# Optimization experiments

Measured on AMD Instinct MI355X. Metric: run time of the kernel, lower is better.

Reference implementation:

```python
import jax, jax.numpy as jnp
import numpy as np


def setup_inputs() -> dict:
    key = jax.random.key(0)
    k1, k2, k3, k4 = jax.random.split(key, 4)
    B, S, D, F = 16, 4096, 1024, 1024
    x = jax.random.normal(k1, (B, S, D), dtype=jnp.float32)
    # Keras 'normal' initializer ~ N(0, 0.05); scale similarly for realism
    W_key = jax.random.normal(k2, (D, F), dtype=jnp.float32) * 0.05
    W_query = jax.random.normal(k3, (D, F), dtype=jnp.float32) * 0.05
    W_value = jax.random.normal(k4, (D, F), dtype=jnp.float32) * 0.05
    return {"x": x, "W_key": W_key, "W_query": W_query, "W_value": W_value}


def reference(x, W_key, W_query, W_value):
    # x: [B,S,D]; W_*: [D,F]
    keys = jnp.tanh(jnp.einsum("bsd,df->bsf", x, W_key))
    query = jnp.tanh(jnp.einsum("bsd,df->bsf", x, W_query))
    value = jnp.tanh(jnp.einsum("bsd,df->bsf", x, W_value))
    # diag(Q K^T) == per-token dot product, computed directly in O(S*F)
    attn_scores = jnp.einsum("bsf,bsf->bs", query, keys)  # [B,S]
    attn_softmax = jax.nn.softmax(attn_scores, axis=-1)[..., None]  # [B,S,1]
    # value^T @ softmax -> [B,F,1]
    weighted_input = jnp.einsum("bsf,bso->bfo", value, attn_softmax)
    return weighted_input, attn_softmax
```

## Files before the change

kernel.cpp:

```cpp
#include <hip/hip_runtime.h>
#include <hip/hip_bf16.h>
#include <math.h>
#include <stdint.h>

typedef _Float16 f16;
typedef _Float16 half8 __attribute__((ext_vector_type(8)));
typedef float f32x4 __attribute__((ext_vector_type(4)));

#define B_ 16
#define S_ 4096
#define D_ 1024
#define F_ 1024
#define TOK (B_*S_)
#define TB2 256
#define FB 128
#define NFB (F_/FB)
#define BK2 64
#define NT (D_/BK2)
#define NS 16
#define CS (S_/NS)

__device__ __forceinline__ void gload_lds16(const void* g, void* l) {
    __builtin_amdgcn_global_load_lds(
        (__attribute__((address_space(1))) const unsigned int*)(unsigned long long)(uintptr_t)g,
        (__attribute__((address_space(3))) unsigned int*)(unsigned int)(uintptr_t)l,
        16, 0, 0);
}

__device__ __forceinline__ void fma4(float4& a, float s, const float4& wv) {
    a.x += s * wv.x; a.y += s * wv.y; a.z += s * wv.z; a.w += s * wv.w;
}
__device__ __forceinline__ void wtanh4(float4& acc, float pw, const float4& a) {
    acc.x += pw * tanhf(a.x); acc.y += pw * tanhf(a.y);
    acc.z += pw * tanhf(a.z); acc.w += pw * tanhf(a.w);
}

__global__ void cvt_x(const float* __restrict__ x, f16* __restrict__ xh) {
    size_t i = ((size_t)blockIdx.x * 256 + threadIdx.x) * 8;
    float4 a = *(const float4*)(x + i);
    float4 b = *(const float4*)(x + i + 4);
    half8 h = {(f16)a.x,(f16)a.y,(f16)a.z,(f16)a.w,
               (f16)b.x,(f16)b.y,(f16)b.z,(f16)b.w};
    *(half8*)(xh + i) = h;
}

__global__ void cvt_w(const float* __restrict__ Wk, const float* __restrict__ Wq,
                      f16* __restrict__ wt) {
    __shared__ float tile[32][33];
    const float* W = (blockIdx.z == 0) ? Wk : Wq;
    f16* outp = wt + (size_t)blockIdx.z * D_ * F_;
    int x0 = blockIdx.x * 32, y0 = blockIdx.y * 32;
    int tx = threadIdx.x, ty = threadIdx.y;
#pragma unroll
    for (int i = 0; i < 4; i++)
        tile[ty + i*8][tx] = W[(size_t)(y0 + ty + i*8) * F_ + x0 + tx];
    __syncthreads();
#pragma unroll
    for (int i = 0; i < 4; i++)
        outp[(size_t)(x0 + ty + i*8) * D_ + y0 + tx] = (f16)tile[tx][ty + i*8];
}

__launch_bounds__(512, 2)
__global__ void score_gemm(const f16* __restrict__ xh, const f16* __restrict__ wt,
                           float* __restrict__ part) {
    __shared__ __align__(16) f16 Xs[2][TB2][BK2];
    __shared__ __align__(16) f16 Ks[2][FB][BK2];
    __shared__ __align__(16) f16 Qs[2][FB][BK2];
    __shared__ float sred[2][TB2];

    const int f0   = blockIdx.x * FB;
    const int tok0 = blockIdx.y * TB2;
    const int t    = threadIdx.x;
    const int lane = t & 63;
    const int w    = t >> 6;
    const int wr   = (w >> 1) * 64;
    const int wc   = (w & 1) * 64;

    const f16* wK = wt + (size_t)f0 * D_;
    const f16* wQ = wt + (size_t)D_ * F_ + (size_t)f0 * D_;

#define STAGE(bi, k0) do {                                                         \
        char* xb = (char*)Xs[bi] + w * 1024;                                       \
        char* kb = (char*)Ks[bi] + w * 1024;                                       \
        char* qb = (char*)Qs[bi] + w * 1024;                                       \
        _Pragma("unroll")                                                          \
        for (int i_ = 0; i_ < 4; ++i_) {                                           \
            int c_ = i_ * 512 + t;                                                 \
            gload_lds16(xh + (size_t)(tok0 + (c_ >> 3)) * D_ + (k0) + (c_ & 7) * 8,\
                        xb + i_ * 8192);                                           \
        }                                                                          \
        _Pragma("unroll")                                                          \
        for (int i_ = 0; i_ < 2; ++i_) {                                           \
            int c_ = i_ * 512 + t;                                                 \
            gload_lds16(wK + (size_t)(c_ >> 3) * D_ + (k0) + (c_ & 7) * 8,         \
                        kb + i_ * 8192);                                           \
            gload_lds16(wQ + (size_t)(c_ >> 3) * D_ + (k0) + (c_ & 7) * 8,         \
                        qb + i_ * 8192);                                           \
        }                                                                          \
    } while (0)

    f32x4 accQ[4][4] = {};
    f32x4 accK[4][4] = {};

    STAGE(0, 0);
    __syncthreads();
    int cur = 0;

    for (int kt = 0; kt < NT; ++kt) {
        if (kt + 1 < NT) STAGE(cur ^ 1, (kt + 1) * BK2);

#pragma unroll
        for (int ks = 0; ks < 2; ++ks) {
            half8 aF[4], bKf[4], bQf[4];
#pragma unroll
            for (int m = 0; m < 4; ++m)
                aF[m] = *(const half8*)&Xs[cur][wr + m * 16 + (lane & 15)][ks * 32 + (lane >> 4) * 8];
#pragma unroll
            for (int n = 0; n < 4; ++n) {
                bKf[n] = *(const half8*)&Ks[cur][wc + n * 16 + (lane & 15)][ks * 32 + (lane >> 4) * 8];
                bQf[n] = *(const half8*)&Qs[cur][wc + n * 16 + (lane & 15)][ks * 32 + (lane >> 4) * 8];
            }
#pragma unroll
            for (int n = 0; n < 4; ++n)
#pragma unroll
                for (int m = 0; m < 4; ++m) {
                    accK[m][n] = __builtin_amdgcn_mfma_f32_16x16x32_f16(aF[m], bKf[n], accK[m][n], 0, 0, 0);
                    accQ[m][n] = __builtin_amdgcn_mfma_f32_16x16x32_f16(aF[m], bQf[n], accQ[m][n], 0, 0, 0);
                }
        }
        __syncthreads();
        cur ^= 1;
    }
#undef STAGE

#pragma unroll
    for (int m = 0; m < 4; ++m) {
        float s[4] = {0.f, 0.f, 0.f, 0.f};
#pragma unroll
        for (int n = 0; n < 4; ++n)
#pragma unroll
            for (int j = 0; j < 4; ++j)
                s[j] += tanhf(accQ[m][n][j]) * tanhf(accK[m][n][j]);
#pragma unroll
        for (int j = 0; j < 4; ++j) {
            s[j] += __shfl_xor(s[j], 1);
            s[j] += __shfl_xor(s[j], 2);
            s[j] += __shfl_xor(s[j], 4);
            s[j] += __shfl_xor(s[j], 8);
        }
        if ((lane & 15) == 0) {
            int g = lane >> 4;
#pragma unroll
            for (int j = 0; j < 4; ++j)
                sred[w & 1][wr + m * 16 + g * 4 + j] = s[j];
        }
    }
    __syncthreads();
    if (t < TB2)
        part[(size_t)blockIdx.x * TOK + tok0 + t] = sred[0][t] + sred[1][t];
}

__global__ void softmax_k(const float* __restrict__ part, float* __restrict__ out) {
    __shared__ float sc[S_];
    __shared__ float red[256];
    const int b = blockIdx.x, t = threadIdx.x;
    float lmax = -1e30f;
    for (int i = t; i < S_; i += 256) {
        float s = 0.f;
#pragma unroll
        for (int fb = 0; fb < NFB; ++fb) s += part[(size_t)fb * TOK + b * S_ + i];
        sc[i] = s;
        lmax = fmaxf(lmax, s);
    }
    red[t] = lmax; __syncthreads();
    for (int o = 128; o > 0; o >>= 1) { if (t < o) red[t] = fmaxf(red[t], red[t + o]); __syncthreads(); }
    const float mx = red[0]; __syncthreads();
    float lsum = 0.f;
    for (int i = t; i < S_; i += 256) { float e = expf(sc[i] - mx); sc[i] = e; lsum += e; }
    red[t] = lsum; __syncthreads();
    for (int o = 128; o > 0; o >>= 1) { if (t < o) red[t] += red[t + o]; __syncthreads(); }
    const float inv = 1.0f / red[0];
    for (int i = t; i < S_; i += 256)
        out[(size_t)B_ * F_ + (size_t)b * S_ + i] = sc[i] * inv;
}

__launch_bounds__(256)
__global__ void value_k3(const float* __restrict__ x, const float* __restrict__ Wv,
                         const float* __restrict__ p_in, float* __restrict__ vpart) {
    __shared__ __align__(16) float xs[4][D_];
    __shared__ float ps[CS];
    __shared__ int   idxs[CS];
    __shared__ int   wsum[4];
    const int b = blockIdx.x, c = blockIdx.y;
    const int t = threadIdx.x, lane = t & 63, w = t >> 6;
    const int s0 = c * CS;

    float p = p_in[(size_t)b * S_ + s0 + t];
    bool flag = p > 1e-7f;
    unsigned long long mask = __ballot(flag);
    if (lane == 0) wsum[w] = __popcll(mask);
    __syncthreads();
    int base = 0;
#pragma unroll
    for (int i = 0; i < 4; ++i) if (i < w) base += wsum[i];
    const int cnt = wsum[0] + wsum[1] + wsum[2] + wsum[3];
    if (flag) {
        int pos = base + __popcll(mask & ((1ull << lane) - 1ull));
        idxs[pos] = s0 + t;
        ps[pos] = p;
    }
    __syncthreads();

    float4 acc = {0.f, 0.f, 0.f, 0.f};
    for (int g = 0; g < cnt; g += 4) {
        __syncthreads();
#pragma unroll
        for (int r = 0; r < 4; ++r) {
            float4 v = {0.f, 0.f, 0.f, 0.f};
            if (g + r < cnt)
                v = ((const float4*)(x + ((size_t)b * S_ + idxs[g + r]) * D_))[t];
            ((float4*)xs[r])[t] = v;
        }
        __syncthreads();
        float4 a0 = {0,0,0,0}, a1 = {0,0,0,0}, a2 = {0,0,0,0}, a3 = {0,0,0,0};
#pragma unroll 2
        for (int dq = 0; dq < D_ / 4; ++dq) {
            const float* wr = Wv + (size_t)dq * 4 * F_;
            float4 wv0 = ((const float4*)(wr        ))[t];
            float4 wv1 = ((const float4*)(wr + F_   ))[t];
            float4 wv2 = ((const float4*)(wr + 2*F_ ))[t];
            float4 wv3 = ((const float4*)(wr + 3*F_ ))[t];
            float4 x0 = ((const float4*)xs[0])[dq];
            float4 x1 = ((const float4*)xs[1])[dq];
            float4 x2 = ((const float4*)xs[2])[dq];
            float4 x3 = ((const float4*)xs[3])[dq];
            fma4(a0, x0.x, wv0); fma4(a0, x0.y, wv1); fma4(a0, x0.z, wv2); fma4(a0, x0.w, wv3);
            fma4(a1, x1.x, wv0); fma4(a1, x1.y, wv1); fma4(a1, x1.z, wv2); fma4(a1, x1.w, wv3);
            fma4(a2, x2.x, wv0); fma4(a2, x2.y, wv1); fma4(a2, x2.z, wv2); fma4(a2, x2.w, wv3);
            fma4(a3, x3.x, wv0); fma4(a3, x3.y, wv1); fma4(a3, x3.z, wv2); fma4(a3, x3.w, wv3);
        }
        int rem = cnt - g;
        if (rem > 0) wtanh4(acc, ps[g + 0], a0);
        if (rem > 1) wtanh4(acc, ps[g + 1], a1);
        if (rem > 2) wtanh4(acc, ps[g + 2], a2);
        if (rem > 3) wtanh4(acc, ps[g + 3], a3);
    }
    ((float4*)(vpart + ((size_t)c * B_ + b) * F_))[t] = acc;
}

__global__ void value_red(const float* __restrict__ vpart, float* __restrict__ out) {
    int i = blockIdx.x * 256 + threadIdx.x;
    float s = 0.f;
#pragma unroll
    for (int c = 0; c < NS; ++c) s += vpart[(size_t)c * B_ * F_ + i];
    out[i] = s;
}

extern "C" void kernel_launch(void* const* d_in, const int* in_sizes, int n_in,
                              void* d_out, int out_size, void* d_ws, size_t ws_size,
                              hipStream_t stream) {
    const float* x  = (const float*)d_in[0];
    const float* Wk = (const float*)d_in[1];
    const float* Wq = (const float*)d_in[2];
    const float* Wv = (const float*)d_in[3];
    float* out = (float*)d_out;
    char* ws = (char*)d_ws;

    f16*   xh   = (f16*)ws;
    f16*   wt   = (f16*)(ws + (size_t)TOK * D_ * 2);
    float* part = (float*)(ws + (size_t)TOK * D_ * 2 + 2 * (size_t)D_ * F_ * 2);

    cvt_x<<<TOK * D_ / 8 / 256, 256, 0, stream>>>(x, xh);
    cvt_w<<<dim3(32, 32, 2), dim3(32, 8), 0, stream>>>(Wk, Wq, wt);
    score_gemm<<<dim3(NFB, TOK / TB2), 512, 0, stream>>>(xh, wt, part);
    softmax_k<<<B_, 256, 0, stream>>>(part, out);
    float* vpart = part;
    const float* p_in = out + (size_t)B_ * F_;
    value_k3<<<dim3(B_, NS), 256, 0, stream>>>(x, Wv, p_in, vpart);
    value_red<<<B_ * F_ / 256, 256, 0, stream>>>(vpart, out);
}
```

Measured before the change: 649.9 us.

## Deepen score GEMM pipeline to four LDS stages with swizzle and block remap

Rewrites the score GEMM main loop to use a 4-slot LDS ring with K-step 32 and three tiles in flight, waited on with explicit vmcnt counts and a single barrier per step. X and weight loads are split so they interleave with the K and Q MFMA groups, and MFMA sections run at raised wave priority. An XOR swizzle on the LDS layout is meant to avoid bank conflicts, and block indices are remapped so that consecutive blocks share the same token tile for L2 reuse. The manual vmcnt accounting is fragile, and halving the K step doubles the number of barriers.

```diff
diff --git a/kernel.cpp b/kernel.cpp
--- a/kernel.cpp
+++ b/kernel.cpp
@@ -15,8 +15,8 @@
 #define TB2 256
 #define FB 128
 #define NFB (F_/FB)
-#define BK2 64
-#define NT (D_/BK2)
+#define BK3 32
+#define NT3 (D_/BK3)
 #define NS 16
 #define CS (S_/NS)
 
@@ -63,13 +63,17 @@
 __launch_bounds__(512, 2)
 __global__ void score_gemm(const f16* __restrict__ xh, const f16* __restrict__ wt,
                            float* __restrict__ part) {
-    __shared__ __align__(16) f16 Xs[2][TB2][BK2];
-    __shared__ __align__(16) f16 Ks[2][FB][BK2];
-    __shared__ __align__(16) f16 Qs[2][FB][BK2];
+    __shared__ __align__(16) f16 Xs[4][TB2 * BK3];
+    __shared__ __align__(16) f16 Ks[4][FB * BK3];
+    __shared__ __align__(16) f16 Qs[4][FB * BK3];
     __shared__ float sred[2][TB2];
 
-    const int f0   = blockIdx.x * FB;
-    const int tok0 = blockIdx.y * TB2;
+    const int hid  = blockIdx.x + blockIdx.y * NFB;
+    const int orig = (hid & 7) * 256 + (hid >> 3);
+    const int fb   = orig & 7;
+    const int f0   = fb * FB;
+    const int tok0 = (orig >> 3) * TB2;
+
     const int t    = threadIdx.x;
     const int lane = t & 63;
     const int w    = t >> 6;
@@ -79,59 +83,100 @@
     const f16* wK = wt + (size_t)f0 * D_;
     const f16* wQ = wt + (size_t)D_ * F_ + (size_t)f0 * D_;
 
-#define STAGE(bi, k0) do {                                                         \
-        char* xb = (char*)Xs[bi] + w * 1024;                                       \
-        char* kb = (char*)Ks[bi] + w * 1024;                                       \
-        char* qb = (char*)Qs[bi] + w * 1024;                                       \
-        _Pragma("unroll")                                                          \
-        for (int i_ = 0; i_ < 4; ++i_) {                                           \
-            int c_ = i_ * 512 + t;                                                 \
-            gload_lds16(xh + (size_t)(tok0 + (c_ >> 3)) * D_ + (k0) + (c_ & 7) * 8,\
-                        xb + i_ * 8192);                                           \
-        }                                                                          \
-        _Pragma("unroll")                                                          \
-        for (int i_ = 0; i_ < 2; ++i_) {                                           \
-            int c_ = i_ * 512 + t;                                                 \
-            gload_lds16(wK + (size_t)(c_ >> 3) * D_ + (k0) + (c_ & 7) * 8,         \
-                        kb + i_ * 8192);                                           \
-            gload_lds16(wQ + (size_t)(c_ >> 3) * D_ + (k0) + (c_ & 7) * 8,         \
-                        qb + i_ * 8192);                                           \
-        }                                                                          \
+    const int cX0 = t, cX1 = t + 512;
+    const int rX0 = cX0 >> 2, rX1 = cX1 >> 2;
+    const int qX0 = (cX0 & 3) ^ ((rX0 >> 1) & 3);
+    const int qX1 = (cX1 & 3) ^ ((rX1 >> 1) & 3);
+    const f16* srcX0 = xh + (size_t)(tok0 + rX0) * D_ + qX0 * 8;
+    const f16* srcX1 = xh + (size_t)(tok0 + rX1) * D_ + qX1 * 8;
+    const int rW = t >> 2;
+    const int qW = (t & 3) ^ ((rW >> 1) & 3);
+    const f16* srcK = wK + (size_t)rW * D_ + qW * 8;
+    const f16* srcQ = wQ + (size_t)rW * D_ + qW * 8;
+    const int wbase = w * 1024;
+
+    int offA[4], offB[4];
+#pragma unroll
+    for (int m = 0; m < 4; ++m) {
+        int row = wr + m * 16 + (lane & 15);
+        int q   = (lane >> 4) ^ ((row >> 1) & 3);
+        offA[m] = row * 32 + q * 8;
+    }
+#pragma unroll
+    for (int n = 0; n < 4; ++n) {
+        int row = wc + n * 16 + (lane & 15);
+        int q   = (lane >> 4) ^ ((row >> 1) & 3);
+        offB[n] = row * 32 + q * 8;
+    }
+
+#define STAGE_X(slot, kof) do {                                   \
+        char* xb = (char*)Xs[slot] + wbase;                       \
+        gload_lds16(srcX0 + (kof), xb);                           \
+        gload_lds16(srcX1 + (kof), xb + 8192);                    \
+    } while (0)
+#define STAGE_W(slot, kof) do {                                   \
+        gload_lds16(srcK + (kof), (char*)Ks[slot] + wbase);       \
+        gload_lds16(srcQ + (kof), (char*)Qs[slot] + wbase);       \
     } while (0)
 
     f32x4 accQ[4][4] = {};
     f32x4 accK[4][4] = {};
 
-    STAGE(0, 0);
-    __syncthreads();
-    int cur = 0;
-
-    for (int kt = 0; kt < NT; ++kt) {
-        if (kt + 1 < NT) STAGE(cur ^ 1, (kt + 1) * BK2);
-
-#pragma unroll
-        for (int ks = 0; ks < 2; ++ks) {
-            half8 aF[4], bKf[4], bQf[4];
+    STAGE_X(0, 0);  STAGE_W(0, 0);
+    STAGE_X(1, 32); STAGE_W(1, 32);
+    STAGE_X(2, 64); STAGE_W(2, 64);
+    asm volatile("s_waitcnt vmcnt(8)" ::: "memory");
+    __builtin_amdgcn_s_barrier();
+    __builtin_amdgcn_sched_barrier(0);
+
+    for (int kt = 0; kt < NT3; ++kt) {
+        const int slot  = kt & 3;
+        const int pslot = (kt + 3) & 3;
+        const int kof   = (kt + 3) * BK3;
+        const f16* Xb = Xs[slot];
+        const f16* Kb = Ks[slot];
+        const f16* Qb = Qs[slot];
+
+        if (kt < NT3 - 3) STAGE_X(pslot, kof);
+        half8 aF[4], bKf[4];
+#pragma unroll
+        for (int m = 0; m < 4; ++m) aF[m]  = *(const half8*)(Xb + offA[m]);
+#pragma unroll
+        for (int n = 0; n < 4; ++n) bKf[n] = *(const half8*)(Kb + offB[n]);
+        __builtin_amdgcn_s_setprio(1);
+#pragma unroll
+        for (int n = 0; n < 4; ++n)
 #pragma unroll
             for (int m = 0; m < 4; ++m)
-                aF[m] = *(const half8*)&Xs[cur][wr + m * 16 + (lane & 15)][ks * 32 + (lane >> 4) * 8];
-#pragma unroll
-            for (int n = 0; n < 4; ++n) {
-                bKf[n] = *(const half8*)&Ks[cur][wc + n * 16 + (lane & 15)][ks * 32 + (lane >> 4) * 8];
-                bQf[n] = *(const half8*)&Qs[cur][wc + n * 16 + (lane & 15)][ks * 32 + (lane >> 4) * 8];
-            }
-#pragma unroll
-            for (int n = 0; n < 4; ++n)
-#pragma unroll
-                for (int m = 0; m < 4; ++m) {
-                    accK[m][n] = __builtin_amdgcn_mfma_f32_16x16x32_f16(aF[m], bKf[n], accK[m][n], 0, 0, 0);
-                    accQ[m][n] = __builtin_amdgcn_mfma_f32_16x16x32_f16(aF[m], bQf[n], accQ[m][n], 0, 0, 0);
-                }
-        }
-        __syncthreads();
-        cur ^= 1;
-    }
-#undef STAGE
+                accK[m][n] = __builtin_amdgcn_mfma_f32_16x16x32_f16(aF[m], bKf[n], accK[m][n], 0, 0, 0);
+        __builtin_amdgcn_s_setprio(0);
+
+        if (kt < NT3 - 3) STAGE_W(pslot, kof);
+        half8 bQf[4];
+#pragma unroll
+        for (int n = 0; n < 4; ++n) bQf[n] = *(const half8*)(Qb + offB[n]);
+        __builtin_amdgcn_s_setprio(1);
+#pragma unroll
+        for (int n = 0; n < 4; ++n)
+#pragma unroll
+            for (int m = 0; m < 4; ++m)
+                accQ[m][n] = __builtin_amdgcn_mfma_f32_16x16x32_f16(aF[m], bQf[n], accQ[m][n], 0, 0, 0);
+        __builtin_amdgcn_s_setprio(0);
+
+        if (kt < NT3 - 3) {
+            asm volatile("s_waitcnt vmcnt(8)" ::: "memory");
+        } else if (kt == NT3 - 3) {
+            asm volatile("s_waitcnt vmcnt(4)" ::: "memory");
+        } else if (kt == NT3 - 2) {
+            asm volatile("s_waitcnt vmcnt(0)" ::: "memory");
+        }
+        if (kt < NT3 - 1) {
+            __builtin_amdgcn_s_barrier();
+            __builtin_amdgcn_sched_barrier(0);
+        }
+    }
+#undef STAGE_X
+#undef STAGE_W
 
 #pragma unroll
     for (int m = 0; m < 4; ++m) {
@@ -157,7 +202,7 @@
     }
     __syncthreads();
     if (t < TB2)
-        part[(size_t)blockIdx.x * TOK + tok0 + t] = sred[0][t] + sred[1][t];
+        part[(size_t)fb * TOK + tok0 + t] = sred[0][t] + sred[1][t];
 }
 
 __global__ void softmax_k(const float* __restrict__ part, float* __restrict__ out) {
```

Result: faster. 634.8 us (-2.3%).
